# Kernel tuning notes

Measured on AMD Instinct MI355X. Metric: run time of the kernel, lower is better.

## Reference

```python
import jax, jax.numpy as jnp
import numpy as np
from math import factorial


def _su2_cg(j1, j2, j3, m1, m2, m3):
    # Complex SU(2) Clebsch-Gordan coefficient <j1 m1; j2 m2 | j3 m3> (Condon-Shortley),
    # same formula as e3nn's _su2_clebsch_gordan_coeff.
    if m3 != m1 + m2:
        return 0.0
    f = factorial
    vmin = max(-j1 + j2 + m3, -j1 + m1, 0)
    vmax = min(j2 + j3 + m1, j3 - j1 + j2, j3 + m3)
    C = ((2 * j3 + 1) * f(j3 + j1 - j2) * f(j3 - j1 + j2) * f(j1 + j2 - j3) / f(j1 + j2 + j3 + 1)
         * f(j3 + m3) * f(j3 - m3) / (f(j1 - m1) * f(j1 + m1) * f(j2 - m2) * f(j2 + m2))) ** 0.5
    S = 0.0
    for v in range(vmin, vmax + 1):
        S += (-1.0) ** (v + j2 + m2) / f(v) * f(j2 + j3 + m1 - v) * f(j1 - m1 + v) / (
            f(j3 - j1 + j2 - v) * f(j3 + m3 - v) * f(v + j1 - j2 - m3))
    return C * S


def _q(l):
    # Change of basis real -> complex spherical harmonics (e3nn convention).
    q = np.zeros((2 * l + 1, 2 * l + 1), dtype=np.complex128)
    for m in range(-l, 0):
        q[l + m, l + abs(m)] = 1 / 2 ** 0.5
        q[l + m, l - abs(m)] = -1j / 2 ** 0.5
    q[l, l] = 1
    for m in range(1, l + 1):
        q[l + m, l + abs(m)] = (-1) ** m / 2 ** 0.5
        q[l + m, l - abs(m)] = 1j * (-1) ** m / 2 ** 0.5
    return (-1j) ** l * q


def _w3j(l1, l2, l3):
    # Real Wigner-3j-like invariant tensor, Frobenius norm 1 (e3nn wigner_3j).
    C = np.zeros((2 * l1 + 1, 2 * l2 + 1, 2 * l3 + 1), dtype=np.complex128)
    for m1 in range(-l1, l1 + 1):
        for m2 in range(-l2, l2 + 1):
            m3 = m1 + m2
            if -l3 <= m3 <= l3:
                C[l1 + m1, l2 + m2, l3 + m3] = _su2_cg(l1, l2, l3, m1, m2, m3)
    C = np.einsum('ij,kl,mn,ikn->jlm', _q(l1), _q(l2), np.conj(_q(l3).T), C)
    C = np.real(C)
    return C / np.linalg.norm(C)


def _cg_full():
    # 1o x 1o -> 0e + 1e + 2e. e3nn FullTensorProduct ('uuu', component norm,
    # element path norm, mul=1) gives path_weight = sqrt(2*l_out + 1) per path.
    return np.concatenate([(2 * l + 1) ** 0.5 * _w3j(1, 1, l) for l in range(3)],
                          axis=-1).astype(np.float32)  # [3, 3, 9]


def setup_inputs() -> dict:
    key = jax.random.key(0)
    N = 8388608  # 2**23 rows, ~96 MB input
    frac = jax.random.normal(key, (N, 3), dtype=jnp.float32)
    cg = jnp.asarray(_cg_full())  # [3, 3, 9] fixed Clebsch-Gordan constants
    return {"frac": frac, "cg": cg}


def reference(frac, cg):
    # SimpleTP.forward: tp(frac, frac) -> [N, 9], then sum over dim 0 -> [9].
    # Fused segment-wise CG contraction + batch reduction in one einsum.
    return jnp.einsum('ni,nj,ijk->k', frac, frac, cg)
```

## Files before the change

kernel.cpp:

```cpp
#include <hip/hip_runtime.h>


constexpr int BLK  = 256;
constexpr int GRID = 1024;
constexpr int WPB  = BLK / 64;
constexpr long NWAVES = (long)GRID * WPB;

#define ACC6(x, y, z)                                              \
    do {                                                           \
        s00 = fmaf((x), (x), s00); s01 = fmaf((x), (y), s01);      \
        s02 = fmaf((x), (z), s02); s11 = fmaf((y), (y), s11);      \
        s12 = fmaf((y), (z), s12); s22 = fmaf((z), (z), s22);      \
    } while (0)

__global__ __launch_bounds__(BLK) void tp_partial(const float* __restrict__ frac,
                                                  float* __restrict__ ws,
                                                  long nchunks) {
    const int  lane = threadIdx.x & 63;
    const int  w    = threadIdx.x >> 6;
    const long wglb = (long)blockIdx.x * WPB + w;
    const float4* __restrict__ f4 = reinterpret_cast<const float4*>(frac);

    float s00 = 0.f, s01 = 0.f, s02 = 0.f, s11 = 0.f, s12 = 0.f, s22 = 0.f;

    #pragma unroll 2
    for (long c = wglb; c < nchunks; c += NWAVES) {
        const long base = c * 768 + lane * 3;
        float4 v[12];
        #pragma unroll
        for (int s = 0; s < 4; ++s)
            #pragma unroll
            for (int k = 0; k < 3; ++k)
                v[s * 3 + k] = f4[base + 192 * s + k];

        #pragma unroll
        for (int s = 0; s < 4; ++s) {
            const float4 a = v[s * 3 + 0];
            const float4 b = v[s * 3 + 1];
            const float4 d = v[s * 3 + 2];
            ACC6(a.x, a.y, a.z);
            ACC6(a.w, b.x, b.y);
            ACC6(b.z, b.w, d.x);
            ACC6(d.y, d.z, d.w);
        }
    }

    #pragma unroll
    for (int off = 32; off > 0; off >>= 1) {
        s00 += __shfl_down(s00, off);
        s01 += __shfl_down(s01, off);
        s02 += __shfl_down(s02, off);
        s11 += __shfl_down(s11, off);
        s12 += __shfl_down(s12, off);
        s22 += __shfl_down(s22, off);
    }

    __shared__ float red[WPB][6];
    if (lane == 0) {
        red[w][0] = s00; red[w][1] = s01; red[w][2] = s02;
        red[w][3] = s11; red[w][4] = s12; red[w][5] = s22;
    }
    __syncthreads();
    if (threadIdx.x < 6) {
        float v = red[0][threadIdx.x] + red[1][threadIdx.x]
                + red[2][threadIdx.x] + red[3][threadIdx.x];
        ws[threadIdx.x * GRID + blockIdx.x] = v;
    }
}

__global__ __launch_bounds__(BLK) void tp_final(const float* __restrict__ frac,
                                                const float* __restrict__ ws,
                                                const float* __restrict__ cg,
                                                float* __restrict__ out,
                                                long tail_row, long nrows) {
    const float4* __restrict__ w4 = reinterpret_cast<const float4*>(ws);
    constexpr int Q = GRID / 4;

    float s[6];
    #pragma unroll
    for (int c = 0; c < 6; ++c) {
        float4 a = w4[c * Q + threadIdx.x];
        s[c] = (a.x + a.y) + (a.z + a.w);
    }

    for (long r = tail_row + threadIdx.x; r < nrows; r += BLK) {
        float x = frac[3 * r + 0], y = frac[3 * r + 1], z = frac[3 * r + 2];
        s[0] = fmaf(x, x, s[0]); s[1] = fmaf(x, y, s[1]); s[2] = fmaf(x, z, s[2]);
        s[3] = fmaf(y, y, s[3]); s[4] = fmaf(y, z, s[4]); s[5] = fmaf(z, z, s[5]);
    }

    #pragma unroll
    for (int off = 32; off > 0; off >>= 1) {
        #pragma unroll
        for (int c = 0; c < 6; ++c) s[c] += __shfl_down(s[c], off);
    }

    __shared__ float red[BLK / 64][6];
    const int lane = threadIdx.x & 63;
    const int wave = threadIdx.x >> 6;
    if (lane == 0) {
        #pragma unroll
        for (int c = 0; c < 6; ++c) red[wave][c] = s[c];
    }
    __syncthreads();

    __shared__ float M[9];
    if (threadIdx.x == 0) {
        float t[6];
        #pragma unroll
        for (int c = 0; c < 6; ++c)
            t[c] = red[0][c] + red[1][c] + red[2][c] + red[3][c];
        M[0] = t[0];  M[1] = t[1];  M[2] = t[2];
        M[3] = t[1];  M[4] = t[3];  M[5] = t[4];
        M[6] = t[2];  M[7] = t[4];  M[8] = t[5];
    }
    __syncthreads();

    if (threadIdx.x < 9) {
        const int k = threadIdx.x;
        float acc = 0.f;
        #pragma unroll
        for (int p = 0; p < 9; ++p)
            acc = fmaf(M[p], cg[p * 9 + k], acc);
        out[k] = acc;
    }
}

extern "C" void kernel_launch(void* const* d_in, const int* in_sizes, int n_in,
                              void* d_out, int out_size, void* d_ws, size_t ws_size,
                              hipStream_t stream) {
    const float* frac = (const float*)d_in[0];
    const float* cg   = (const float*)d_in[1];
    float*       out  = (float*)d_out;
    float*       ws   = (float*)d_ws;

    const long nfloats  = in_sizes[0];
    const long nrows    = nfloats / 3;
    const long nchunks  = nfloats / 3072;
    const long tail_row = nchunks * 1024;

    tp_partial<<<GRID, BLK, 0, stream>>>(frac, ws, nchunks);
    tp_final<<<1, BLK, 0, stream>>>(frac, ws, cg, out, tail_row, nrows);
}
```

Measured before the change: 24.38 us.

## Fuse partial and final reduction kernels via last-block atomic counter

Merges the two-kernel reduction into one kernel. Each block writes its partials with atomics and increments a global counter, and the last block to arrive does the final reduction, the tail rows and the CG contraction. This removes the second launch and its dependency gap, though a memset launch is added to reset the counter. The grid roughly doubles to 2032 blocks and the unroll-2 pragma is dropped, which changes memory-level parallelism. The relaxed-ordering atomics could be a memory-visibility risk.

Measured after the change: 44.61 us. 1.83x slower.

```diff
diff --git a/kernel.cpp b/kernel.cpp
--- a/kernel.cpp
+++ b/kernel.cpp
@@ -2,7 +2,7 @@
 
 
 constexpr int BLK  = 256;
-constexpr int GRID = 1024;
+constexpr int GRID = 2032;
 constexpr int WPB  = BLK / 64;
 constexpr long NWAVES = (long)GRID * WPB;
 
@@ -13,17 +13,22 @@
         s12 = fmaf((y), (z), s12); s22 = fmaf((z), (z), s22);      \
     } while (0)
 
-__global__ __launch_bounds__(BLK) void tp_partial(const float* __restrict__ frac,
-                                                  float* __restrict__ ws,
-                                                  long nchunks) {
+__global__ __launch_bounds__(BLK) void tp_fused(const float* __restrict__ frac,
+                                                float* __restrict__ ws,
+                                                const float* __restrict__ cg,
+                                                float* __restrict__ out,
+                                                long nchunks, long tail_row,
+                                                long nrows) {
     const int  lane = threadIdx.x & 63;
     const int  w    = threadIdx.x >> 6;
     const long wglb = (long)blockIdx.x * WPB + w;
     const float4* __restrict__ f4 = reinterpret_cast<const float4*>(frac);
 
+    float* __restrict__ part = ws + 8;
+    unsigned* counter = reinterpret_cast<unsigned*>(ws);
+
     float s00 = 0.f, s01 = 0.f, s02 = 0.f, s11 = 0.f, s12 = 0.f, s22 = 0.f;
 
-    #pragma unroll 2
     for (long c = wglb; c < nchunks; c += NWAVES) {
         const long base = c * 768 + lane * 3;
         float4 v[12];
@@ -56,33 +61,36 @@
     }
 
     __shared__ float red[WPB][6];
+    __shared__ int   is_last;
     if (lane == 0) {
         red[w][0] = s00; red[w][1] = s01; red[w][2] = s02;
         red[w][3] = s11; red[w][4] = s12; red[w][5] = s22;
     }
     __syncthreads();
+
     if (threadIdx.x < 6) {
         float v = red[0][threadIdx.x] + red[1][threadIdx.x]
                 + red[2][threadIdx.x] + red[3][threadIdx.x];
-        ws[threadIdx.x * GRID + blockIdx.x] = v;
+        __hip_atomic_exchange(&part[threadIdx.x * GRID + blockIdx.x], v,
+                              __ATOMIC_RELAXED, __HIP_MEMORY_SCOPE_AGENT);
     }
-}
+    __syncthreads();
 
-__global__ __launch_bounds__(BLK) void tp_final(const float* __restrict__ frac,
-                                                const float* __restrict__ ws,
-                                                const float* __restrict__ cg,
-                                                float* __restrict__ out,
-                                                long tail_row, long nrows) {
-    const float4* __restrict__ w4 = reinterpret_cast<const float4*>(ws);
-    constexpr int Q = GRID / 4;
+    if (threadIdx.x == 0) {
+        unsigned old = __hip_atomic_fetch_add(counter, 1u, __ATOMIC_RELAXED,
+                                              __HIP_MEMORY_SCOPE_AGENT);
+        is_last = (old == GRID - 1) ? 1 : 0;
+    }
+    __syncthreads();
+    if (!is_last) return;
 
-    float s[6];
-    #pragma unroll
-    for (int c = 0; c < 6; ++c) {
-        float4 a = w4[c * Q + threadIdx.x];
-        s[c] = (a.x + a.y) + (a.z + a.w);
+    float s[6] = {0.f, 0.f, 0.f, 0.f, 0.f, 0.f};
+    for (int b = threadIdx.x; b < GRID; b += BLK) {
+        #pragma unroll
+        for (int c = 0; c < 6; ++c)
+            s[c] += __hip_atomic_load(&part[c * GRID + b],
+                                      __ATOMIC_RELAXED, __HIP_MEMORY_SCOPE_AGENT);
     }
-
     for (long r = tail_row + threadIdx.x; r < nrows; r += BLK) {
         float x = frac[3 * r + 0], y = frac[3 * r + 1], z = frac[3 * r + 2];
         s[0] = fmaf(x, x, s[0]); s[1] = fmaf(x, y, s[1]); s[2] = fmaf(x, z, s[2]);
@@ -94,34 +102,29 @@
         #pragma unroll
         for (int c = 0; c < 6; ++c) s[c] += __shfl_down(s[c], off);
     }
-
-    __shared__ float red[BLK / 64][6];
-    const int lane = threadIdx.x & 63;
-    const int wave = threadIdx.x >> 6;
     if (lane == 0) {
         #pragma unroll
-        for (int c = 0; c < 6; ++c) red[wave][c] = s[c];
+        for (int c = 0; c < 6; ++c) red[w][c] = s[c];
     }
     __syncthreads();
 
-    __shared__ float M[9];
+    __shared__ float fin[6 + 9];
+    if (threadIdx.x < 6)
+        fin[threadIdx.x] = red[0][threadIdx.x] + red[1][threadIdx.x]
+                         + red[2][threadIdx.x] + red[3][threadIdx.x];
+    __syncthreads();
     if (threadIdx.x == 0) {
-        float t[6];
-        #pragma unroll
-        for (int c = 0; c < 6; ++c)
-            t[c] = red[0][c] + red[1][c] + red[2][c] + red[3][c];
-        M[0] = t[0];  M[1] = t[1];  M[2] = t[2];
-        M[3] = t[1];  M[4] = t[3];  M[5] = t[4];
-        M[6] = t[2];  M[7] = t[4];  M[8] = t[5];
+        fin[6 + 0] = fin[0]; fin[6 + 1] = fin[1]; fin[6 + 2] = fin[2];
+        fin[6 + 3] = fin[1]; fin[6 + 4] = fin[3]; fin[6 + 5] = fin[4];
+        fin[6 + 6] = fin[2]; fin[6 + 7] = fin[4]; fin[6 + 8] = fin[5];
     }
     __syncthreads();
-
     if (threadIdx.x < 9) {
         const int k = threadIdx.x;
         float acc = 0.f;
         #pragma unroll
         for (int p = 0; p < 9; ++p)
-            acc = fmaf(M[p], cg[p * 9 + k], acc);
+            acc = fmaf(fin[6 + p], cg[p * 9 + k], acc);
         out[k] = acc;
     }
 }
@@ -139,6 +142,6 @@
     const long nchunks  = nfloats / 3072;
     const long tail_row = nchunks * 1024;
 
-    tp_partial<<<GRID, BLK, 0, stream>>>(frac, ws, nchunks);
-    tp_final<<<1, BLK, 0, stream>>>(frac, ws, cg, out, tail_row, nrows);
+    hipMemsetAsync(d_ws, 0, 4, stream);
+    tp_fused<<<GRID, BLK, 0, stream>>>(frac, ws, cg, out, nchunks, tail_row, nrows);
 }
```
